# Performance work log

Measured on AMD Instinct MI355X. Metric: run time of the kernel, lower is better.

The kernel has to match this reference:

```python
import jax, jax.numpy as jnp
import numpy as np
import math

INPUT_SIZE = 128
HIDDEN_SIZE = 64
MEM_DIM = 64
B, S = 8, 2048


def _xavier(key, shape):
    fan_in, fan_out = shape[0], shape[1]
    a = math.sqrt(6.0 / (fan_in + fan_out))
    return jax.random.uniform(key, shape, jnp.float32, minval=-a, maxval=a)


def setup_inputs() -> dict:
    key = jax.random.key(0)
    ks = jax.random.split(key, 8)
    x = jax.random.normal(ks[0], (B, S, INPUT_SIZE), jnp.float32)
    return {
        "x": x,
        "c_prev": jnp.zeros((MEM_DIM, MEM_DIM), jnp.float32),
        "n_prev": jnp.zeros((MEM_DIM, 1), jnp.float32),
        "w_q": _xavier(ks[1], (INPUT_SIZE, HIDDEN_SIZE)),
        "b_q": jnp.zeros((HIDDEN_SIZE,), jnp.float32),
        "w_k": _xavier(ks[2], (INPUT_SIZE, MEM_DIM)),
        "b_k": jnp.zeros((MEM_DIM,), jnp.float32),
        "w_v": _xavier(ks[3], (INPUT_SIZE, MEM_DIM)),
        "b_v": jnp.zeros((MEM_DIM,), jnp.float32),
        "w_i": _xavier(ks[4], (INPUT_SIZE, 1)),
        "b_i": jnp.zeros((1,), jnp.float32),
        "w_f": _xavier(ks[5], (INPUT_SIZE, 1)),
        "b_f": jnp.zeros((1,), jnp.float32),
        "w_o": _xavier(ks[6], (INPUT_SIZE, HIDDEN_SIZE)),
        "b_o": jnp.zeros((HIDDEN_SIZE,), jnp.float32),
    }


def reference(x, c_prev, n_prev, w_q, b_q, w_k, b_k, w_v, b_v,
              w_i, b_i, w_f, b_f, w_o, b_o):
    b, s, d = x.shape
    mem_dim = w_k.shape[1]
    xf = x.reshape(b * s, d)  # [T, D], T = B*S

    q_t = xf @ w_q + b_q                                   # [T, H]
    k_t = (xf @ w_k + b_k) * (1.0 / math.sqrt(mem_dim))    # [T, M]
    v_t = xf @ w_v + b_v                                   # [T, M]
    i_t = jnp.exp(xf @ w_i + b_i)                          # [T, 1]
    f_t = jax.nn.sigmoid(xf @ w_f + b_f)                   # [T, 1]

    # Faithful to source: c_prev / n_prev are NEVER updated in the loop,
    # so every step mixes the same initial state -> fully parallel.
    # c_t[t] = f[t] * c_prev + i[t] * outer(v[t], k[t])
    c_t = (f_t[:, :, None] * c_prev[None]
           + i_t[:, :, None] * v_t[:, :, None] * k_t[:, None, :])  # [T, M, M]
    # n_t[t] = f[t] * n_prev + i[t] * k[t][:, None]
    n_t = f_t[:, :, None] * n_prev[None] + i_t[:, :, None] * k_t[:, :, None]  # [T, M, 1]

    c_t = c_t.reshape(b, s, mem_dim, mem_dim)
    n_t = n_t.reshape(b, s, mem_dim, 1)
    qv = q_t.reshape(b, s, mem_dim)  # requires hidden_size == mem_dim

    nq = jnp.einsum("bsm,bsm->bs", n_t[..., 0], qv)
    max_nqt = jnp.maximum(jnp.abs(nq), 1.0)                # [B, S]
    h_tilde = jnp.einsum("bsmk,bsk->bsm", c_t, qv) / max_nqt[..., None]

    o_t = jax.nn.sigmoid(xf @ w_o + b_o).reshape(b, s, -1)
    h_t = o_t * h_tilde                                    # [B, S, H]
    return (h_t, c_t, n_t)
```

## Files before the change

kernel.cpp:

```cpp
#include <hip/hip_runtime.h>
#include <cstdint>

#define NTOK 16384

typedef float f4 __attribute__((ext_vector_type(4)));
typedef __attribute__((ext_vector_type(4))) float f32x4;
typedef __attribute__((ext_vector_type(8))) short bf16x8;

__device__ __forceinline__ float readlane_f(float v, int lane) {
  return __int_as_float(__builtin_amdgcn_readlane(__float_as_int(v), lane));
}

__device__ __forceinline__ float wave_sum64(float v) {
  #pragma unroll
  for (int s = 1; s < 64; s <<= 1) v += __shfl_xor(v, s, 64);
  return v;
}

__device__ __forceinline__ float half_sum32(float v) {
  #pragma unroll
  for (int s = 1; s < 32; s <<= 1) v += __shfl_xor(v, s, 64);
  return v;
}

__device__ __forceinline__ uint32_t rne_bf16(float f) {
  uint32_t u = __float_as_uint(f);
  return (u + 0x7FFFu + ((u >> 16) & 1u)) >> 16;
}

__global__ void __launch_bounds__(512, 2)
fused_kernel(const float* __restrict__ x,
             const float* __restrict__ c_prev,
             const float* __restrict__ n_prev,
             const float* __restrict__ w_q, const float* __restrict__ b_q,
             const float* __restrict__ w_k, const float* __restrict__ b_k,
             const float* __restrict__ w_v, const float* __restrict__ b_v,
             const float* __restrict__ w_i, const float* __restrict__ b_i,
             const float* __restrict__ w_f, const float* __restrict__ b_f,
             const float* __restrict__ w_o, const float* __restrict__ b_o,
             float* __restrict__ h_out,
             float* __restrict__ c_out,
             float* __restrict__ n_out)
{
  __shared__ uint32_t smem[16384];
  __shared__ float    cp[64][65];
  __shared__ float    hbuf[4096];
  __shared__ float    nbuf[4096];
  const int tid  = threadIdx.x;
  const int lane = tid & 63;
  const int wid  = tid >> 6;
  const int T0   = blockIdx.x * 64;

  {
    const int n   = tid & 255;
    const int col = n & 63;
    const float* W = (n < 128) ? ((n < 64) ? w_q : w_k)
                               : ((n < 192) ? w_v : w_o);
    const int kph = tid >> 8;
    #pragma unroll
    for (int it = 0; it < 32; ++it) {
      const int kp = it * 2 + kph;
      const float a = W[(2 * kp)     * 64 + col];
      const float b = W[(2 * kp + 1) * 64 + col];
      const uint32_t pk = rne_bf16(a) | (rne_bf16(b) << 16);
      const int unit = (n << 4) + ((kp >> 2) ^ (n & 15));
      smem[(unit << 2) + (kp & 3)] = pk;
    }
  }
  for (int idx = tid; idx < 4096; idx += 512)
    cp[idx >> 6][idx & 63] = c_prev[idx];

  const f4* xp = (const f4*)(x + (size_t)(T0 + wid * 8) * 128);
  f4 xc[4];
  xc[0] = xp[lane];
  xc[1] = xp[64 + lane];
  xc[2] = xp[128 + lane];
  xc[3] = xp[192 + lane];

  __syncthreads();

  const int mt  = wid & 3;
  const int ntg = (wid >> 2) * 8;
  bf16x8 afrag[4];
  {
    const float* xr = x + (size_t)(T0 + mt * 16 + (lane & 15)) * 128
                        + ((lane >> 4) * 8);
    #pragma unroll
    for (int ks = 0; ks < 4; ++ks) {
      const f4 lo = *(const f4*)(xr + ks * 32);
      const f4 hi = *(const f4*)(xr + ks * 32 + 4);
      union { uint32_t u[4]; bf16x8 v; } cv;
      cv.u[0] = rne_bf16(lo.x) | (rne_bf16(lo.y) << 16);
      cv.u[1] = rne_bf16(lo.z) | (rne_bf16(lo.w) << 16);
      cv.u[2] = rne_bf16(hi.x) | (rne_bf16(hi.y) << 16);
      cv.u[3] = rne_bf16(hi.z) | (rne_bf16(hi.w) << 16);
      afrag[ks] = cv.v;
    }
  }
  f32x4 acc[8];
  #pragma unroll
  for (int j = 0; j < 8; ++j) acc[j] = (f32x4){0.f, 0.f, 0.f, 0.f};
  {
    const int bsub = lane & 15, bh = lane >> 4;
    #pragma unroll
    for (int nti = 0; nti < 8; ++nti) {
      const int n = (ntg + nti) * 16 + bsub;
      #pragma unroll
      for (int ks = 0; ks < 4; ++ks) {
        const int unit = (n << 4) + ((ks * 4 + bh) ^ (n & 15));
        const bf16x8 bfrag = *(const bf16x8*)&smem[unit << 2];
        acc[nti] = __builtin_amdgcn_mfma_f32_16x16x32_bf16(afrag[ks], bfrag,
                                                           acc[nti], 0, 0, 0);
      }
    }
  }
  __syncthreads();
  {
    float* y = (float*)smem;
    const int trow = mt * 16 + (lane >> 4) * 4;
    const int fcol = lane & 15;
    #pragma unroll
    for (int nti = 0; nti < 8; ++nti) {
      const int f = (ntg + nti) * 16 + fcol;
      #pragma unroll
      for (int r = 0; r < 4; ++r)
        y[(trow + r) * 256 + f] = acc[nti][r];
    }
  }
  __syncthreads();

  float itv[8], ftv[8];
  {
    const int dbase = (lane & 31) << 2;
    const f4 wi4 = *(const f4*)&w_i[dbase];
    const f4 wf4 = *(const f4*)&w_f[dbase];
    const float sbi = b_i[0], sbf = b_f[0];
    #pragma unroll
    for (int c = 0; c < 4; ++c) {
      float pi = xc[c].x * wi4.x + xc[c].y * wi4.y + xc[c].z * wi4.z + xc[c].w * wi4.w;
      float pf = xc[c].x * wf4.x + xc[c].y * wf4.y + xc[c].z * wf4.z + xc[c].w * wf4.w;
      pi = half_sum32(pi);
      pf = half_sum32(pf);
      itv[2 * c]     = __expf(readlane_f(pi, 0)  + sbi);
      itv[2 * c + 1] = __expf(readlane_f(pi, 32) + sbi);
      ftv[2 * c]     = 1.0f / (1.0f + __expf(-(readlane_f(pf, 0)  + sbf)));
      ftv[2 * c + 1] = 1.0f / (1.0f + __expf(-(readlane_f(pf, 32) + sbf)));
    }
  }

  const float bq = b_q[lane], bk = b_k[lane], bv = b_v[lane], bo = b_o[lane];
  const float npv = n_prev[lane];
  const int   m   = lane & 15;
  const float* y  = (const float*)smem;

  #pragma unroll 1
  for (int tt = 0; tt < 8; ++tt) {
    const int    tl = wid * 8 + tt;
    const size_t t  = (size_t)(T0 + tl);
    const float q   = y[tl * 256 + lane] + bq;
    const float k   = (y[tl * 256 + 64 + lane] + bk) * 0.125f;
    const float v   = y[tl * 256 + 128 + lane] + bv;
    const float oz  = y[tl * 256 + 192 + lane] + bo;
    const float it_ = itv[tt];
    const float ft_ = ftv[tt];

    const float iv = it_ * v;
    const float k40 = __shfl(k, 4 * m, 64);
    const float k41 = __shfl(k, 4 * m + 1, 64);
    const float k42 = __shfl(k, 4 * m + 2, 64);
    const float k43 = __shfl(k, 4 * m + 3, 64);
    float ivr[16];
    #pragma unroll
    for (int s = 0; s < 16; ++s)
      ivr[s] = __shfl(iv, 4 * ((s + 2 * wid) & 15) + (lane >> 4), 64);

    f4* ct = (f4*)(c_out + t * 4096);
    #pragma unroll
    for (int s = 0; s < 16; ++s) {
      const int ss  = (s + 2 * wid) & 15;
      const int row = 4 * ss + (lane >> 4);
      const f4 c4 = *(const f4*)&cp[row][4 * m];
      f4 val;
      val.x = fmaf(ft_, c4.x, ivr[s] * k40);
      val.y = fmaf(ft_, c4.y, ivr[s] * k41);
      val.z = fmaf(ft_, c4.z, ivr[s] * k42);
      val.w = fmaf(ft_, c4.w, ivr[s] * k43);
      ct[ss * 64 + lane] = val;
    }

    const float n_val = fmaf(ft_, npv, it_ * k);
    nbuf[tl * 64 + lane] = n_val;

    const float nq = wave_sum64(n_val * q);
    const float kq = wave_sum64(k * q);

    float c0 = 0.f, c1 = 0.f, c2 = 0.f, c3 = 0.f;
    #pragma unroll
    for (int j = 0; j < 16; ++j) {
      const f4 r4 = *(const f4*)&cp[lane][4 * j];
      c0 = fmaf(r4.x, readlane_f(q, 4 * j),     c0);
      c1 = fmaf(r4.y, readlane_f(q, 4 * j + 1), c1);
      c2 = fmaf(r4.z, readlane_f(q, 4 * j + 2), c2);
      c3 = fmaf(r4.w, readlane_f(q, 4 * j + 3), c3);
    }
    const float cpq = (c0 + c1) + (c2 + c3);

    const float o    = 1.0f / (1.0f + __expf(-oz));
    const float inv  = 1.0f / fmaxf(fabsf(nq), 1.0f);
    const float htil = fmaf(ft_, cpq, it_ * v * kq) * inv;
    hbuf[tl * 64 + lane] = o * htil;
  }

  {
    const float* hb = hbuf + wid * 512 + lane * 8;
    const float* nb = nbuf + wid * 512 + lane * 8;
    const size_t base = (size_t)(T0 + wid * 8) * 64 + lane * 8;
    f4 h0 = {hb[0], hb[1], hb[2], hb[3]};
    f4 h1 = {hb[4], hb[5], hb[6], hb[7]};
    f4 n0 = {nb[0], nb[1], nb[2], nb[3]};
    f4 n1 = {nb[4], nb[5], nb[6], nb[7]};
    *(f4*)(h_out + base)     = h0;
    *(f4*)(h_out + base + 4) = h1;
    *(f4*)(n_out + base)     = n0;
    *(f4*)(n_out + base + 4) = n1;
  }
}

extern "C" void kernel_launch(void* const* d_in, const int* in_sizes, int n_in,
                              void* d_out, int out_size, void* d_ws, size_t ws_size,
                              hipStream_t stream) {
  const float* x      = (const float*)d_in[0];
  const float* c_prev = (const float*)d_in[1];
  const float* n_prev = (const float*)d_in[2];
  const float* w_q = (const float*)d_in[3];
  const float* b_q = (const float*)d_in[4];
  const float* w_k = (const float*)d_in[5];
  const float* b_k = (const float*)d_in[6];
  const float* w_v = (const float*)d_in[7];
  const float* b_v = (const float*)d_in[8];
  const float* w_i = (const float*)d_in[9];
  const float* b_i = (const float*)d_in[10];
  const float* w_f = (const float*)d_in[11];
  const float* b_f = (const float*)d_in[12];
  const float* w_o = (const float*)d_in[13];
  const float* b_o = (const float*)d_in[14];

  float* h_out = (float*)d_out;
  float* c_out = h_out + 1048576;
  float* n_out = c_out + 67108864;

  fused_kernel<<<256, 512, 0, stream>>>(x, c_prev, n_prev,
                                        w_q, b_q, w_k, b_k, w_v, b_v,
                                        w_i, b_i, w_f, b_f, w_o, b_o,
                                        h_out, c_out, n_out);
}
```

Measured before the change: 56.80 us.

## Split c_t outer-product expansion into a separate grid-wide streaming kernel

```diff
diff --git a/kernel.cpp b/kernel.cpp
--- a/kernel.cpp
+++ b/kernel.cpp
@@ -29,18 +29,20 @@
 }
 
 __global__ void __launch_bounds__(512, 2)
-fused_kernel(const float* __restrict__ x,
-             const float* __restrict__ c_prev,
-             const float* __restrict__ n_prev,
-             const float* __restrict__ w_q, const float* __restrict__ b_q,
-             const float* __restrict__ w_k, const float* __restrict__ b_k,
-             const float* __restrict__ w_v, const float* __restrict__ b_v,
-             const float* __restrict__ w_i, const float* __restrict__ b_i,
-             const float* __restrict__ w_f, const float* __restrict__ b_f,
-             const float* __restrict__ w_o, const float* __restrict__ b_o,
-             float* __restrict__ h_out,
-             float* __restrict__ c_out,
-             float* __restrict__ n_out)
+proj_kernel(const float* __restrict__ x,
+            const float* __restrict__ c_prev,
+            const float* __restrict__ n_prev,
+            const float* __restrict__ w_q, const float* __restrict__ b_q,
+            const float* __restrict__ w_k, const float* __restrict__ b_k,
+            const float* __restrict__ w_v, const float* __restrict__ b_v,
+            const float* __restrict__ w_i, const float* __restrict__ b_i,
+            const float* __restrict__ w_f, const float* __restrict__ b_f,
+            const float* __restrict__ w_o, const float* __restrict__ b_o,
+            float* __restrict__ h_out,
+            float* __restrict__ n_out,
+            float* __restrict__ k_buf,
+            float* __restrict__ iv_buf,
+            float* __restrict__ ft_buf)
 {
   __shared__ uint32_t smem[16384];
   __shared__ float    cp[64][65];
@@ -150,7 +152,6 @@
 
   const float bq = b_q[lane], bk = b_k[lane], bv = b_v[lane], bo = b_o[lane];
   const float npv = n_prev[lane];
-  const int   m   = lane & 15;
   const float* y  = (const float*)smem;
 
   #pragma unroll 1
@@ -164,29 +165,9 @@
     const float it_ = itv[tt];
     const float ft_ = ftv[tt];
 
-    const float iv = it_ * v;
-    const float k40 = __shfl(k, 4 * m, 64);
-    const float k41 = __shfl(k, 4 * m + 1, 64);
-    const float k42 = __shfl(k, 4 * m + 2, 64);
-    const float k43 = __shfl(k, 4 * m + 3, 64);
-    float ivr[16];
-    #pragma unroll
-    for (int s = 0; s < 16; ++s)
-      ivr[s] = __shfl(iv, 4 * ((s + 2 * wid) & 15) + (lane >> 4), 64);
-
-    f4* ct = (f4*)(c_out + t * 4096);
-    #pragma unroll
-    for (int s = 0; s < 16; ++s) {
-      const int ss  = (s + 2 * wid) & 15;
-      const int row = 4 * ss + (lane >> 4);
-      const f4 c4 = *(const f4*)&cp[row][4 * m];
-      f4 val;
-      val.x = fmaf(ft_, c4.x, ivr[s] * k40);
-      val.y = fmaf(ft_, c4.y, ivr[s] * k41);
-      val.z = fmaf(ft_, c4.z, ivr[s] * k42);
-      val.w = fmaf(ft_, c4.w, ivr[s] * k43);
-      ct[ss * 64 + lane] = val;
-    }
+    k_buf[t * 64 + lane]  = k;
+    iv_buf[t * 64 + lane] = it_ * v;
+    if (lane == 0) ft_buf[t] = ft_;
 
     const float n_val = fmaf(ft_, npv, it_ * k);
     nbuf[tl * 64 + lane] = n_val;
@@ -223,6 +204,34 @@
     *(f4*)(h_out + base + 4) = h1;
     *(f4*)(n_out + base)     = n0;
     *(f4*)(n_out + base + 4) = n1;
+  }
+}
+
+__global__ void __launch_bounds__(256)
+expand_kernel(const float* __restrict__ c_prev,
+              const float* __restrict__ k_buf,
+              const float* __restrict__ iv_buf,
+              const float* __restrict__ ft_buf,
+              float* __restrict__ c_out)
+{
+  const uint32_t nthreads = 2048 * 256;
+  uint32_t gid = blockIdx.x * 256 + threadIdx.x;
+  f4* __restrict__ out = (f4*)c_out;
+  #pragma unroll 4
+  for (int it = 0; it < 32; ++it, gid += nthreads) {
+    const uint32_t t  = gid >> 10;
+    const uint32_t r  = (gid >> 4) & 63;
+    const uint32_t c4 = gid & 15;
+    const float ft = ft_buf[t];
+    const float iv = iv_buf[(t << 6) | r];
+    const f4 kk = *(const f4*)&k_buf[(t << 6) | (c4 << 2)];
+    const f4 cp = *(const f4*)&c_prev[(r << 6) | (c4 << 2)];
+    f4 val;
+    val.x = fmaf(ft, cp.x, iv * kk.x);
+    val.y = fmaf(ft, cp.y, iv * kk.y);
+    val.z = fmaf(ft, cp.z, iv * kk.z);
+    val.w = fmaf(ft, cp.w, iv * kk.w);
+    out[gid] = val;
   }
 }
 
@@ -249,8 +258,13 @@
   float* c_out = h_out + 1048576;
   float* n_out = c_out + 67108864;
 
-  fused_kernel<<<256, 512, 0, stream>>>(x, c_prev, n_prev,
-                                        w_q, b_q, w_k, b_k, w_v, b_v,
-                                        w_i, b_i, w_f, b_f, w_o, b_o,
-                                        h_out, c_out, n_out);
-}
+  float* k_buf  = (float*)d_ws;
+  float* iv_buf = k_buf + 1048576;
+  float* ft_buf = iv_buf + 1048576;
+
+  proj_kernel<<<256, 512, 0, stream>>>(x, c_prev, n_prev,
+                                       w_q, b_q, w_k, b_k, w_v, b_v,
+                                       w_i, b_i, w_f, b_f, w_o, b_o,
+                                       h_out, n_out, k_buf, iv_buf, ft_buf);
+  expand_kernel<<<2048, 256, 0, stream>>>(c_prev, k_buf, iv_buf, ft_buf, c_out);
+}
```

Measured after the change: 72.70 us. +28.0%, slower.
